# Kernel tuning notes

Hardware: AMD Instinct MI355X
Metric: run time of the kernel (lower is better)

The kernel has to match this reference:

```python
import jax, jax.numpy as jnp
import numpy as np


def _segmented_exclusive_cumsum(vals, seg_start_flags):
    """Exclusive cumsum of vals that resets at segment starts (flags True)."""
    def combine(a, b):
        va, fa = a
        vb, fb = b
        return (jnp.where(fb, vb, va + vb), fa | fb)
    inclusive, _ = jax.lax.associative_scan(combine, (vals, seg_start_flags))
    return inclusive - vals


def setup_inputs() -> dict:
    key = jax.random.key(0)
    k1, k2 = jax.random.split(key)
    n_rays = 65536
    samples_per_ray = 128  # average; ragged via sorted random ray ids
    n_pts = n_rays * samples_per_ray  # 8_388_608 sample points
    density = jax.random.normal(k1, (n_pts,), dtype=jnp.float32)
    ray_id = jnp.sort(jax.random.randint(k2, (n_pts,), 0, n_rays)).astype(jnp.int32)
    shift = jnp.float32(-3.0)      # self.act_shift
    interval = jnp.float32(0.5)    # stepsize * voxel_size_ratio
    return {"density": density, "shift": shift, "interval": interval,
            "ray_id": ray_id, "n_rays": n_rays}


def reference(density, shift, interval, ray_id, n_rays):
    # Raw2Alpha: alpha = 1 - exp(-softplus(density + shift) * interval)
    # log(1 - alpha) = -interval * softplus(density + shift)  (stable, no log of tiny)
    log_one_minus_alpha = -interval * jax.nn.softplus(density + shift)
    alpha = 1.0 - jnp.exp(log_one_minus_alpha)

    # Alphas2Weights: per-ray exclusive cumprod of (1 - alpha) in log space.
    # ray_id is sorted; segment starts where the ray id changes.
    seg_start = jnp.concatenate(
        [jnp.ones((1,), dtype=bool), ray_id[1:] != ray_id[:-1]])
    log_T = _segmented_exclusive_cumsum(log_one_minus_alpha, seg_start)
    T = jnp.exp(log_T)                      # transmittance before each sample
    weights = alpha * T                     # [n_pts]

    # alphainv_last[r] = prod over ray r of (1 - alpha) = residual transmittance
    log_total = jax.ops.segment_sum(log_one_minus_alpha, ray_id,
                                    num_segments=n_rays)
    alphainv_last = jnp.exp(log_total)      # [n_rays]; empty rays -> exp(0)=1
    return weights, alphainv_last
```

## Files before the change

kernel.cpp:

```cpp
#include <hip/hip_runtime.h>
#include <math.h>


#define LOG2E 1.4426950408889634f
#define EPT   8
#define WSPAN (64 * EPT)
#define BPTS  (4 * WSPAN)
#define WIN   256
#define WPL   (WIN / 64)
#define NXCD  8

typedef float vf4 __attribute__((ext_vector_type(4)));

__device__ __forceinline__ float exp2f_(float x) { return __builtin_amdgcn_exp2f(x); }
__device__ __forceinline__ float log2f_(float x) { return __builtin_amdgcn_logf(x); }
__device__ __forceinline__ float rsqf_(float x)  { return __builtin_amdgcn_rsqf(x); }

__device__ __forceinline__ float oma(float d, float sh2, float negc, bool fast) {
    const float y = fmaf(d, LOG2E, sh2);
    if (fast) return rsqf_(1.0f + exp2f_(y));
    const float sp = fmaxf(y, 0.f) + log2f_(1.f + exp2f_(-fabsf(y)));
    return exp2f_(negc * sp);
}

template <int CTRL, int RM>
__device__ __forceinline__ void seg_step(float& V, int& F) {
    const int vs_i = __builtin_amdgcn_update_dpp(
        0x3f800000, __builtin_bit_cast(int, V), CTRL, RM, 0xF, false);
    const int fs = __builtin_amdgcn_update_dpp(0, F, CTRL, RM, 0xF, false);
    const float vs = __builtin_bit_cast(float, vs_i);
    V = F ? V : vs * V;
    F = F | fs;
}

__device__ __forceinline__ float wave_prod_bcast(float x) {
#define STEPP(CTRL, RM)                                                        \
    { int t_ = __builtin_amdgcn_update_dpp(0x3f800000,                         \
          __builtin_bit_cast(int, x), CTRL, RM, 0xF, false);                   \
      x *= __builtin_bit_cast(float, t_); }
    STEPP(0x111, 0xF) STEPP(0x112, 0xF) STEPP(0x114, 0xF)
    STEPP(0x118, 0xF) STEPP(0x142, 0xA) STEPP(0x143, 0xC)
#undef STEPP
    return __builtin_bit_cast(float,
        __builtin_amdgcn_readlane(__builtin_bit_cast(int, x), 63));
}

__device__ __forceinline__ int wave_imax_bcast(int x) {
#define STEPM(CTRL, RM)                                                        \
    { int t_ = __builtin_amdgcn_update_dpp((int)0x80000000, x, CTRL, RM,       \
                                           0xF, false);                        \
      x = (x > t_) ? x : t_; }
    STEPM(0x111, 0xF) STEPM(0x112, 0xF) STEPM(0x114, 0xF)
    STEPM(0x118, 0xF) STEPM(0x142, 0xA) STEPM(0x143, 0xC)
#undef STEPM
    return __builtin_amdgcn_readlane(x, 63);
}

__global__ void __launch_bounds__(256)
fused_alpha_weights(const float* __restrict__ density,
                    const int*   __restrict__ ray_id,
                    const float* __restrict__ shift_p,
                    const float* __restrict__ interval_p,
                    float* __restrict__ weights,
                    float* __restrict__ alphainv,
                    int n_pts, int n_rays) {
    const int t    = threadIdx.x;
    const int lane = t & 63;
    const int wid  = t >> 6;

    const int nwg  = gridDim.x;
    const int orig = blockIdx.x;
    const int qq   = nwg / NXCD, rr = nwg % NXCD;
    const int xcd  = orig % NXCD;
    const int blk  = (xcd < rr ? xcd * (qq + 1) : rr * (qq + 1) + (xcd - rr) * qq)
                   + orig / NXCD;

    const int wbase = blk * BPTS + wid * WSPAN;
    if (wbase >= n_pts) return;
    const int idx0  = wbase + lane * EPT;

    const float shift = shift_p[0];
    const float c     = interval_p[0];
    const float sh2   = shift * LOG2E;
    const float negc  = -c;
    const bool  fast  = (c == 0.5f);

    int r[EPT + 1]; float d[EPT]; bool v[EPT];
    if (idx0 + EPT <= n_pts) {
        const int4   ri0 = *reinterpret_cast<const int4*>(ray_id + idx0);
        const int4   ri1 = *reinterpret_cast<const int4*>(ray_id + idx0 + 4);
        const float4 de0 = *reinterpret_cast<const float4*>(density + idx0);
        const float4 de1 = *reinterpret_cast<const float4*>(density + idx0 + 4);
        r[0] = ri0.x; r[1] = ri0.y; r[2] = ri0.z; r[3] = ri0.w;
        r[4] = ri1.x; r[5] = ri1.y; r[6] = ri1.z; r[7] = ri1.w;
        d[0] = de0.x; d[1] = de0.y; d[2] = de0.z; d[3] = de0.w;
        d[4] = de1.x; d[5] = de1.y; d[6] = de1.z; d[7] = de1.w;
        #pragma unroll
        for (int k = 0; k < EPT; ++k) v[k] = true;
    } else {
        #pragma unroll
        for (int k = 0; k < EPT; ++k) {
            const int i = idx0 + k;
            v[k] = (i < n_pts);
            r[k] = v[k] ? ray_id[i] : n_rays;
            d[k] = v[k] ? density[i] : 0.0f;
        }
    }

    int rprev_edge = -1;
    if (lane == 0 && idx0 > 0 && idx0 <= n_pts) rprev_edge = ray_id[idx0 - 1];
    int rnext_edge = n_rays;
    if (lane == 63 && idx0 + EPT < n_pts) rnext_edge = ray_id[idx0 + EPT];

    int   w_id[WPL]; float w_den[WPL];
    int   rfirst = 0;
    if (wbase > 0) {
        rfirst = ray_id[wbase];
        #pragma unroll
        for (int j = 0; j < WPL; ++j) {
            const int wi = wbase - WIN + 64 * j + lane;
            w_id[j]  = ray_id[wi];
            w_den[j] = density[wi];
        }
    }

    const int rp_sh = __shfl_up(r[EPT - 1], 1, 64);
    const int rprev = (lane > 0) ? rp_sh : rprev_edge;
    const int rn_sh = __shfl_down(r[0], 1, 64);
    r[EPT] = (lane < 63) ? rn_sh : rnext_edge;

    float a[EPT]; int f[EPT];
    #pragma unroll
    for (int k = 0; k < EPT; ++k) {
        const float av = oma(d[k], sh2, negc, fast);
        a[k] = v[k] ? av : 1.0f;
        f[k] = (k == 0) ? (r[0] != rprev) : (r[k] != r[k - 1]);
    }

    float V = a[0];  int F = f[0];
    #pragma unroll
    for (int k = 1; k < EPT; ++k) {
        V = f[k] ? a[k] : V * a[k];
        F |= f[k];
    }

    float Vi = V;  int Fi = F;
    seg_step<0x111, 0xF>(Vi, Fi);
    seg_step<0x112, 0xF>(Vi, Fi);
    seg_step<0x114, 0xF>(Vi, Fi);
    seg_step<0x118, 0xF>(Vi, Fi);
    seg_step<0x142, 0xA>(Vi, Fi);
    seg_step<0x143, 0xC>(Vi, Fi);

    float carry0 = 1.0f;
    if (wbase > 0) {
        int cand = -1;
        #pragma unroll
        for (int j = 0; j < WPL; ++j)
            if (w_id[j] != rfirst) cand = 64 * j + lane;
        const int m = wave_imax_bcast(cand);

        float pp = 1.0f;
        #pragma unroll
        for (int j = 0; j < WPL; ++j) {
            const int i = 64 * j + lane;
            const float aa = oma(w_den[j], sh2, negc, fast);
            pp *= (i > m) ? aa : 1.0f;
        }
        carry0 = wave_prod_bcast(pp);

        if (m < 0) {
            int lo = wbase - WIN;
            int mg = -1;
            while (mg < 0) {
                const int wstart = lo - WIN;
                int c2 = -1;
                float pw = 1.0f;
                #pragma unroll
                for (int j = 0; j < WPL; ++j) {
                    const int i = wstart + 64 * j + lane;
                    const int vv = (i >= 0) ? ray_id[i] : -1;
                    if (vv != rfirst) c2 = 64 * j + lane;
                }
                const int m2 = wave_imax_bcast(c2);
                #pragma unroll
                for (int j = 0; j < WPL; ++j) {
                    const int iw = 64 * j + lane;
                    const int i  = wstart + iw;
                    float aa = 1.0f;
                    if (iw > m2 && i >= 0) aa = oma(density[i], sh2, negc, fast);
                    pw *= aa;
                }
                carry0 *= wave_prod_bcast(pw);
                if (m2 >= 0) mg = 1; else lo = wstart;
            }
        }
    }

    float Vx = __shfl_up(Vi, 1, 64);
    int   Fx = __shfl_up(Fi, 1, 64);
    if (lane == 0) { Vx = 1.0f; Fx = 0; }
    const float Ev = Fx ? Vx : carry0 * Vx;

    float T[EPT], e[EPT];
    float prev = Ev;
    #pragma unroll
    for (int k = 0; k < EPT; ++k) {
        T[k] = f[k] ? 1.0f : prev;
        e[k] = T[k] * a[k];
        prev = e[k];
    }

    if (idx0 + EPT <= n_pts) {
        vf4 w0 = { T[0] - e[0], T[1] - e[1], T[2] - e[2], T[3] - e[3] };
        vf4 w1 = { T[4] - e[4], T[5] - e[5], T[6] - e[6], T[7] - e[7] };
        __builtin_nontemporal_store(w0, reinterpret_cast<vf4*>(weights + idx0));
        __builtin_nontemporal_store(w1, reinterpret_cast<vf4*>(weights + idx0 + 4));
    } else {
        #pragma unroll
        for (int k = 0; k < EPT; ++k)
            if (v[k]) weights[idx0 + k] = T[k] - e[k];
    }

    #pragma unroll
    for (int k = 0; k < EPT; ++k) {
        if (v[k] && r[k] != r[k + 1]) {
            alphainv[r[k]] = e[k];
            for (int q = r[k] + 1; q < r[k + 1]; ++q) alphainv[q] = 1.0f;
        }
    }
    if (idx0 == 0) {
        for (int q = 0; q < r[0]; ++q) alphainv[q] = 1.0f;
    }
}

extern "C" void kernel_launch(void* const* d_in, const int* in_sizes, int n_in,
                              void* d_out, int out_size, void* d_ws, size_t ws_size,
                              hipStream_t stream) {
    const float* density  = (const float*)d_in[0];
    const float* shift    = (const float*)d_in[1];
    const float* interval = (const float*)d_in[2];
    const int*   ray_id   = (const int*)d_in[3];
    const int n_pts  = in_sizes[0];
    const int n_rays = out_size - n_pts;

    float* weights  = (float*)d_out;
    float* alphainv = (float*)d_out + n_pts;

    const int grid = (n_pts + BPTS - 1) / BPTS;
    fused_alpha_weights<<<grid, 256, 0, stream>>>(
        density, ray_id, shift, interval, weights, alphainv, n_pts, n_rays);
}
```

Baseline: 22.09 us.

## Process four spans per wave with carried transmittance and double-buffered loads

Each wave now covers four consecutive 512-point spans instead of one. The transmittance carry and previous ray id pass serially from span to span, so the backward window lookback for the carry is paid once per four spans. The next span's loads are issued before the current span is computed, a simple double buffer. In exchange the grid has four times fewer blocks and each wave runs a serial chain of four scans, which lowers parallelism and occupancy on a memory-bound kernel.

```diff
diff --git a/kernel.cpp b/kernel.cpp
--- a/kernel.cpp
+++ b/kernel.cpp
@@ -4,7 +4,9 @@
 
 #define LOG2E 1.4426950408889634f
 #define EPT   8
-#define WSPAN (64 * EPT)
+#define SPAN  (64 * EPT)
+#define NSPAN 4
+#define WSPAN (SPAN * NSPAN)
 #define BPTS  (4 * WSPAN)
 #define WIN   256
 #define WPL   (WIN / 64)
@@ -15,6 +17,11 @@
 __device__ __forceinline__ float exp2f_(float x) { return __builtin_amdgcn_exp2f(x); }
 __device__ __forceinline__ float log2f_(float x) { return __builtin_amdgcn_logf(x); }
 __device__ __forceinline__ float rsqf_(float x)  { return __builtin_amdgcn_rsqf(x); }
+
+__device__ __forceinline__ float readlane_f(float x, int l) {
+    return __builtin_bit_cast(float,
+        __builtin_amdgcn_readlane(__builtin_bit_cast(int, x), l));
+}
 
 __device__ __forceinline__ float oma(float d, float sh2, float negc, bool fast) {
     const float y = fmaf(d, LOG2E, sh2);
@@ -54,6 +61,113 @@
     STEPM(0x118, 0xF) STEPM(0x142, 0xA) STEPM(0x143, 0xC)
 #undef STEPM
     return __builtin_amdgcn_readlane(x, 63);
+}
+
+__device__ __forceinline__ void load_span(
+    const int* __restrict__ ray_id, const float* __restrict__ density,
+    int sb, int lane, int n_pts, int n_rays, int r[EPT], float d[EPT])
+{
+    const int i0 = sb + lane * EPT;
+    if (i0 + EPT <= n_pts) {
+        const int4   ri0 = *reinterpret_cast<const int4*>(ray_id + i0);
+        const int4   ri1 = *reinterpret_cast<const int4*>(ray_id + i0 + 4);
+        const float4 de0 = *reinterpret_cast<const float4*>(density + i0);
+        const float4 de1 = *reinterpret_cast<const float4*>(density + i0 + 4);
+        r[0] = ri0.x; r[1] = ri0.y; r[2] = ri0.z; r[3] = ri0.w;
+        r[4] = ri1.x; r[5] = ri1.y; r[6] = ri1.z; r[7] = ri1.w;
+        d[0] = de0.x; d[1] = de0.y; d[2] = de0.z; d[3] = de0.w;
+        d[4] = de1.x; d[5] = de1.y; d[6] = de1.z; d[7] = de1.w;
+    } else {
+        #pragma unroll
+        for (int k = 0; k < EPT; ++k) {
+            const int i = i0 + k;
+            const bool vv = (i < n_pts);
+            r[k] = vv ? ray_id[i] : n_rays;
+            d[k] = vv ? density[i] : 0.0f;
+        }
+    }
+}
+
+__device__ __forceinline__ void compute_span(
+    const int r[EPT], const float d[EPT], int sb, int lane,
+    int n_pts, int n_rays, float sh2, float negc, bool fast,
+    float carry_in, int rprev_u, int rnext_u,
+    float* __restrict__ weights, float* __restrict__ alphainv,
+    float& carry_out, int& rlast_out)
+{
+    const int idx0 = sb + lane * EPT;
+
+    bool v[EPT];
+    #pragma unroll
+    for (int k = 0; k < EPT; ++k) v[k] = (idx0 + k < n_pts);
+
+    const int rp_sh = __shfl_up(r[EPT - 1], 1, 64);
+    const int rprev = (lane > 0) ? rp_sh : rprev_u;
+    const int rn_sh = __shfl_down(r[0], 1, 64);
+    const int rnext = (lane < 63) ? rn_sh : rnext_u;
+
+    float a[EPT]; int f[EPT];
+    #pragma unroll
+    for (int k = 0; k < EPT; ++k) {
+        const float av = oma(d[k], sh2, negc, fast);
+        a[k] = v[k] ? av : 1.0f;
+        f[k] = (k == 0) ? (r[0] != rprev) : (r[k] != r[k - 1]);
+    }
+
+    float V = a[0];  int F = f[0];
+    #pragma unroll
+    for (int k = 1; k < EPT; ++k) {
+        V = f[k] ? a[k] : V * a[k];
+        F |= f[k];
+    }
+
+    float Vi = V;  int Fi = F;
+    seg_step<0x111, 0xF>(Vi, Fi);
+    seg_step<0x112, 0xF>(Vi, Fi);
+    seg_step<0x114, 0xF>(Vi, Fi);
+    seg_step<0x118, 0xF>(Vi, Fi);
+    seg_step<0x142, 0xA>(Vi, Fi);
+    seg_step<0x143, 0xC>(Vi, Fi);
+
+    float Vx = __shfl_up(Vi, 1, 64);
+    int   Fx = __shfl_up(Fi, 1, 64);
+    if (lane == 0) { Vx = 1.0f; Fx = 0; }
+    const float Ev = Fx ? Vx : carry_in * Vx;
+
+    float T[EPT], e[EPT];
+    float prev = Ev;
+    #pragma unroll
+    for (int k = 0; k < EPT; ++k) {
+        T[k] = f[k] ? 1.0f : prev;
+        e[k] = T[k] * a[k];
+        prev = e[k];
+    }
+
+    if (idx0 + EPT <= n_pts) {
+        vf4 w0 = { T[0] - e[0], T[1] - e[1], T[2] - e[2], T[3] - e[3] };
+        vf4 w1 = { T[4] - e[4], T[5] - e[5], T[6] - e[6], T[7] - e[7] };
+        __builtin_nontemporal_store(w0, reinterpret_cast<vf4*>(weights + idx0));
+        __builtin_nontemporal_store(w1, reinterpret_cast<vf4*>(weights + idx0 + 4));
+    } else {
+        #pragma unroll
+        for (int k = 0; k < EPT; ++k)
+            if (v[k]) weights[idx0 + k] = T[k] - e[k];
+    }
+
+    #pragma unroll
+    for (int k = 0; k < EPT; ++k) {
+        const int rk1 = (k < EPT - 1) ? r[k + 1] : rnext;
+        if (v[k] && r[k] != rk1) {
+            alphainv[r[k]] = e[k];
+            for (int q = r[k] + 1; q < rk1; ++q) alphainv[q] = 1.0f;
+        }
+    }
+    if (idx0 == 0) {
+        for (int q = 0; q < r[0]; ++q) alphainv[q] = 1.0f;
+    }
+
+    carry_out = readlane_f(e[EPT - 1], 63);
+    rlast_out = __builtin_amdgcn_readlane(r[EPT - 1], 63);
 }
 
 __global__ void __launch_bounds__(256)
@@ -75,9 +189,8 @@
     const int blk  = (xcd < rr ? xcd * (qq + 1) : rr * (qq + 1) + (xcd - rr) * qq)
                    + orig / NXCD;
 
-    const int wbase = blk * BPTS + wid * WSPAN;
-    if (wbase >= n_pts) return;
-    const int idx0  = wbase + lane * EPT;
+    const int wb = blk * BPTS + wid * WSPAN;
+    if (wb >= n_pts) return;
 
     const float shift = shift_p[0];
     const float c     = interval_p[0];
@@ -85,75 +198,31 @@
     const float negc  = -c;
     const bool  fast  = (c == 0.5f);
 
-    int r[EPT + 1]; float d[EPT]; bool v[EPT];
-    if (idx0 + EPT <= n_pts) {
-        const int4   ri0 = *reinterpret_cast<const int4*>(ray_id + idx0);
-        const int4   ri1 = *reinterpret_cast<const int4*>(ray_id + idx0 + 4);
-        const float4 de0 = *reinterpret_cast<const float4*>(density + idx0);
-        const float4 de1 = *reinterpret_cast<const float4*>(density + idx0 + 4);
-        r[0] = ri0.x; r[1] = ri0.y; r[2] = ri0.z; r[3] = ri0.w;
-        r[4] = ri1.x; r[5] = ri1.y; r[6] = ri1.z; r[7] = ri1.w;
-        d[0] = de0.x; d[1] = de0.y; d[2] = de0.z; d[3] = de0.w;
-        d[4] = de1.x; d[5] = de1.y; d[6] = de1.z; d[7] = de1.w;
-        #pragma unroll
-        for (int k = 0; k < EPT; ++k) v[k] = true;
-    } else {
-        #pragma unroll
-        for (int k = 0; k < EPT; ++k) {
-            const int i = idx0 + k;
-            v[k] = (i < n_pts);
-            r[k] = v[k] ? ray_id[i] : n_rays;
-            d[k] = v[k] ? density[i] : 0.0f;
-        }
-    }
-
-    int rprev_edge = -1;
-    if (lane == 0 && idx0 > 0 && idx0 <= n_pts) rprev_edge = ray_id[idx0 - 1];
-    int rnext_edge = n_rays;
-    if (lane == 63 && idx0 + EPT < n_pts) rnext_edge = ray_id[idx0 + EPT];
+    int rA[EPT]; float dA[EPT];
+    load_span(ray_id, density, wb, lane, n_pts, n_rays, rA, dA);
 
     int   w_id[WPL]; float w_den[WPL];
     int   rfirst = 0;
-    if (wbase > 0) {
-        rfirst = ray_id[wbase];
+    if (wb > 0) {
+        rfirst = ray_id[wb];
         #pragma unroll
         for (int j = 0; j < WPL; ++j) {
-            const int wi = wbase - WIN + 64 * j + lane;
+            const int wi = wb - WIN + 64 * j + lane;
             w_id[j]  = ray_id[wi];
             w_den[j] = density[wi];
         }
     }
 
-    const int rp_sh = __shfl_up(r[EPT - 1], 1, 64);
-    const int rprev = (lane > 0) ? rp_sh : rprev_edge;
-    const int rn_sh = __shfl_down(r[0], 1, 64);
-    r[EPT] = (lane < 63) ? rn_sh : rnext_edge;
-
-    float a[EPT]; int f[EPT];
-    #pragma unroll
-    for (int k = 0; k < EPT; ++k) {
-        const float av = oma(d[k], sh2, negc, fast);
-        a[k] = v[k] ? av : 1.0f;
-        f[k] = (k == 0) ? (r[0] != rprev) : (r[k] != r[k - 1]);
-    }
-
-    float V = a[0];  int F = f[0];
-    #pragma unroll
-    for (int k = 1; k < EPT; ++k) {
-        V = f[k] ? a[k] : V * a[k];
-        F |= f[k];
-    }
-
-    float Vi = V;  int Fi = F;
-    seg_step<0x111, 0xF>(Vi, Fi);
-    seg_step<0x112, 0xF>(Vi, Fi);
-    seg_step<0x114, 0xF>(Vi, Fi);
-    seg_step<0x118, 0xF>(Vi, Fi);
-    seg_step<0x142, 0xA>(Vi, Fi);
-    seg_step<0x143, 0xC>(Vi, Fi);
-
-    float carry0 = 1.0f;
-    if (wbase > 0) {
+    int rB[EPT]; float dB[EPT];
+    load_span(ray_id, density, wb + SPAN, lane, n_pts, n_rays, rB, dB);
+
+    const int rnext3 = (wb + WSPAN < n_pts) ? ray_id[wb + WSPAN] : n_rays;
+
+    float carry = 1.0f;
+    int   rprev_u = -1;
+    if (wb > 0) {
+        rprev_u = __builtin_amdgcn_readlane(w_id[WPL - 1], 63);
+
         int cand = -1;
         #pragma unroll
         for (int j = 0; j < WPL; ++j)
@@ -167,10 +236,10 @@
             const float aa = oma(w_den[j], sh2, negc, fast);
             pp *= (i > m) ? aa : 1.0f;
         }
-        carry0 = wave_prod_bcast(pp);
+        carry = wave_prod_bcast(pp);
 
         if (m < 0) {
-            int lo = wbase - WIN;
+            int lo = wb - WIN;
             int mg = -1;
             while (mg < 0) {
                 const int wstart = lo - WIN;
@@ -191,47 +260,31 @@
                     if (iw > m2 && i >= 0) aa = oma(density[i], sh2, negc, fast);
                     pw *= aa;
                 }
-                carry0 *= wave_prod_bcast(pw);
+                carry *= wave_prod_bcast(pw);
                 if (m2 >= 0) mg = 1; else lo = wstart;
             }
         }
     }
 
-    float Vx = __shfl_up(Vi, 1, 64);
-    int   Fx = __shfl_up(Fi, 1, 64);
-    if (lane == 0) { Vx = 1.0f; Fx = 0; }
-    const float Ev = Fx ? Vx : carry0 * Vx;
-
-    float T[EPT], e[EPT];
-    float prev = Ev;
-    #pragma unroll
-    for (int k = 0; k < EPT; ++k) {
-        T[k] = f[k] ? 1.0f : prev;
-        e[k] = T[k] * a[k];
-        prev = e[k];
-    }
-
-    if (idx0 + EPT <= n_pts) {
-        vf4 w0 = { T[0] - e[0], T[1] - e[1], T[2] - e[2], T[3] - e[3] };
-        vf4 w1 = { T[4] - e[4], T[5] - e[5], T[6] - e[6], T[7] - e[7] };
-        __builtin_nontemporal_store(w0, reinterpret_cast<vf4*>(weights + idx0));
-        __builtin_nontemporal_store(w1, reinterpret_cast<vf4*>(weights + idx0 + 4));
-    } else {
-        #pragma unroll
-        for (int k = 0; k < EPT; ++k)
-            if (v[k]) weights[idx0 + k] = T[k] - e[k];
-    }
-
-    #pragma unroll
-    for (int k = 0; k < EPT; ++k) {
-        if (v[k] && r[k] != r[k + 1]) {
-            alphainv[r[k]] = e[k];
-            for (int q = r[k] + 1; q < r[k + 1]; ++q) alphainv[q] = 1.0f;
-        }
-    }
-    if (idx0 == 0) {
-        for (int q = 0; q < r[0]; ++q) alphainv[q] = 1.0f;
-    }
+    int rlast;
+
+    compute_span(rA, dA, wb, lane, n_pts, n_rays, sh2, negc, fast,
+                 carry, rprev_u, __builtin_amdgcn_readlane(rB[0], 0),
+                 weights, alphainv, carry, rlast);
+
+    load_span(ray_id, density, wb + 2 * SPAN, lane, n_pts, n_rays, rA, dA);
+    compute_span(rB, dB, wb + SPAN, lane, n_pts, n_rays, sh2, negc, fast,
+                 carry, rlast, __builtin_amdgcn_readlane(rA[0], 0),
+                 weights, alphainv, carry, rlast);
+
+    load_span(ray_id, density, wb + 3 * SPAN, lane, n_pts, n_rays, rB, dB);
+    compute_span(rA, dA, wb + 2 * SPAN, lane, n_pts, n_rays, sh2, negc, fast,
+                 carry, rlast, __builtin_amdgcn_readlane(rB[0], 0),
+                 weights, alphainv, carry, rlast);
+
+    compute_span(rB, dB, wb + 3 * SPAN, lane, n_pts, n_rays, sh2, negc, fast,
+                 carry, rlast, rnext3,
+                 weights, alphainv, carry, rlast);
 }
 
 extern "C" void kernel_launch(void* const* d_in, const int* in_sizes, int n_in,
```

After: 24.84 us. +12.4%, slower.
